# Performance work log

Measured on AMD Instinct MI355X. Metric: run time of the kernel, lower is better.

Reference implementation:

```python
import math
import jax, jax.numpy as jnp
import numpy as np

LMAX = 4
IN_FEATURES = 128
OUT_FEATURES = 128
BATCH = 16384
NUM_M = (LMAX + 1) ** 2  # 25


def setup_inputs() -> dict:
    key = jax.random.key(0)
    k1, k2 = jax.random.split(key)
    bound = 1.0 / math.sqrt(IN_FEATURES)
    input_embedding = jax.random.normal(k1, (BATCH, NUM_M, IN_FEATURES), dtype=jnp.float32)
    # Matches flax initializers.uniform(scale=2*bound): values in [0, 2*bound).
    # The module subtracts `bound` inside __call__, replicated in reference().
    weight = jax.random.uniform(k2, (LMAX + 1, OUT_FEATURES, IN_FEATURES),
                                dtype=jnp.float32, minval=0.0, maxval=2.0 * bound)
    bias = jnp.zeros((OUT_FEATURES,), dtype=jnp.float32)
    return {"input_embedding": input_embedding, "weight": weight, "bias": bias}


def reference(input_embedding, weight, bias):
    in_features = input_embedding.shape[-1]
    bound = 1.0 / math.sqrt(in_features)
    w = weight - bound  # centered weights, shape [lmax+1, out, in]
    lmax = weight.shape[0] - 1
    # expand_index[m] = l such that m lies in degree-l block (2l+1 entries each)
    expand_index = jnp.repeat(jnp.arange(lmax + 1), 2 * jnp.arange(lmax + 1) + 1,
                              total_repeat_length=(lmax + 1) ** 2)
    w_expanded = w[expand_index]  # [(lmax+1)^2, out, in] -- small gather
    out = jnp.einsum('bmi,moi->bmo', input_embedding, w_expanded)
    out = out.at[:, 0, :].add(bias)  # bias only on the l=0 (m=0) component
    return out
```

## Files before the change

kernel.cpp:

```cpp
#include <hip/hip_runtime.h>


#define BATCH 16384
#define NUM_M 25
#define NF 128
#define BB 64
#define ROWS_PER_BLOCK (BATCH / BB)
#define TILE_ROWS 64
#define NIT (ROWS_PER_BLOCK / TILE_ROWS)

typedef __attribute__((ext_vector_type(8))) short short8;
typedef __attribute__((ext_vector_type(4))) float floatx4;

__device__ inline short f2bf(float f) {
    union { float f; unsigned u; } v;
    v.f = f;
    unsigned r = v.u + 0x7fffu + ((v.u >> 16) & 1u);
    return (short)(r >> 16);
}

__device__ inline short8 cvt8(floatx4 x0, floatx4 x1) {
    short8 f;
    f[0] = f2bf(x0[0]); f[1] = f2bf(x0[1]);
    f[2] = f2bf(x0[2]); f[3] = f2bf(x0[3]);
    f[4] = f2bf(x1[0]); f[5] = f2bf(x1[1]);
    f[6] = f2bf(x1[2]); f[7] = f2bf(x1[3]);
    return f;
}

__global__ __launch_bounds__(256, 2)
void so3_mfma_kernel(const float* __restrict__ x,
                     const float* __restrict__ w,
                     const float* __restrict__ bias,
                     float* __restrict__ out) {
    const int m = blockIdx.y;
    const int l = (m >= 16) ? 4 : (m >= 9) ? 3 : (m >= 4) ? 2 : (m >= 1) ? 1 : 0;
    const int wave = threadIdx.x >> 6;
    const int lane = threadIdx.x & 63;
    const int q    = lane >> 4;
    const int n16  = lane & 15;
    const float bound = 0.08838834764831843f;

    short8 wfrag[8][4];
    {
        const float* wl = w + l * NF * NF;
        #pragma unroll
        for (int nt = 0; nt < 8; ++nt) {
            const int o = nt * 16 + n16;
            #pragma unroll
            for (int kc = 0; kc < 4; ++kc) {
                const int k = kc * 32 + q * 8;
                const floatx4* p = (const floatx4*)(wl + o * NF + k);
                floatx4 w0 = p[0], w1 = p[1];
                short8 f;
                f[0] = f2bf(w0[0] - bound); f[1] = f2bf(w0[1] - bound);
                f[2] = f2bf(w0[2] - bound); f[3] = f2bf(w0[3] - bound);
                f[4] = f2bf(w1[0] - bound); f[5] = f2bf(w1[1] - bound);
                f[6] = f2bf(w1[2] - bound); f[7] = f2bf(w1[3] - bound);
                wfrag[nt][kc] = f;
            }
        }
    }

    const int b0 = blockIdx.x * ROWS_PER_BLOCK;
    const int row0 = b0 + wave * 16 + n16;
    const float* xr0  = x   + (row0 * NUM_M + m) * NF;
    float*       or0  = out + (row0 * NUM_M + m) * NF;
    const int tile_stride = TILE_ROWS * NUM_M * NF;

    floatx4 raw[2][8];
    #pragma unroll
    for (int kc = 0; kc < 4; ++kc) {
        const floatx4* p = (const floatx4*)(xr0 + kc * 32 + q * 8);
        raw[0][2 * kc]     = p[0];
        raw[0][2 * kc + 1] = p[1];
    }

    #pragma unroll
    for (int it = 0; it < NIT; ++it) {
        const int cur = it & 1;

        if (it + 1 < NIT) {
            const float* xr = xr0 + (it + 1) * tile_stride;
            #pragma unroll
            for (int kc = 0; kc < 4; ++kc) {
                const floatx4* p = (const floatx4*)(xr + kc * 32 + q * 8);
                raw[cur ^ 1][2 * kc]     = p[0];
                raw[cur ^ 1][2 * kc + 1] = p[1];
            }
        }

        floatx4 acc[8] = {};
        #pragma unroll
        for (int kc = 0; kc < 4; ++kc) {
            const short8 a = cvt8(raw[cur][2 * kc], raw[cur][2 * kc + 1]);
            #pragma unroll
            for (int nt = 0; nt < 8; ++nt) {
                acc[nt] = __builtin_amdgcn_mfma_f32_16x16x32_bf16(
                    wfrag[nt][kc], a, acc[nt], 0, 0, 0);
            }
        }

        float* orow = or0 + it * tile_stride;
        #pragma unroll
        for (int nt = 0; nt < 8; ++nt) {
            floatx4 v = acc[nt];
            if (m == 0) {
                const floatx4 b4 = *(const floatx4*)(bias + nt * 16 + q * 4);
                v[0] += b4[0]; v[1] += b4[1]; v[2] += b4[2]; v[3] += b4[3];
            }
            __builtin_nontemporal_store(v, (floatx4*)(orow + nt * 16 + q * 4));
        }
    }
}

extern "C" void kernel_launch(void* const* d_in, const int* in_sizes, int n_in,
                              void* d_out, int out_size, void* d_ws, size_t ws_size,
                              hipStream_t stream) {
    const float* x    = (const float*)d_in[0];
    const float* w    = (const float*)d_in[1];
    const float* bias = (const float*)d_in[2];
    float* out = (float*)d_out;

    dim3 grid(BB, NUM_M);
    dim3 block(256);
    so3_mfma_kernel<<<grid, block, 0, stream>>>(x, w, bias, out);
}
```

Measured before the change: 416.7 us.

## Stage bf16 weights in swizzled LDS and raise occupancy to four blocks per SIMD

Weight fragments no longer live in registers (32 short8 per thread). Each block now converts its degree-l weight matrix to bf16 once into a 32KB XOR-swizzled LDS buffer and reads the fragments from LDS inside the MFMA loop. The x prefetch double buffer shrinks to a single raw buffer that is converted to bf16 fragments before the next load, and launch bounds go from 2 to 4. The aim is more waves in flight to hide the memory latency of this bandwidth-bound kernel, at the cost of LDS reads on every tile and a block-wide barrier.

```diff
diff --git a/kernel.cpp b/kernel.cpp
--- a/kernel.cpp
+++ b/kernel.cpp
@@ -28,77 +28,91 @@
     return f;
 }
 
-__global__ __launch_bounds__(256, 2)
+__global__ __launch_bounds__(256, 4)
 void so3_mfma_kernel(const float* __restrict__ x,
                      const float* __restrict__ w,
                      const float* __restrict__ bias,
                      float* __restrict__ out) {
+    __shared__ short wlds[NF * NF];
+
     const int m = blockIdx.y;
     const int l = (m >= 16) ? 4 : (m >= 9) ? 3 : (m >= 4) ? 2 : (m >= 1) ? 1 : 0;
-    const int wave = threadIdx.x >> 6;
-    const int lane = threadIdx.x & 63;
+    const int tid  = threadIdx.x;
+    const int wave = tid >> 6;
+    const int lane = tid & 63;
     const int q    = lane >> 4;
     const int n16  = lane & 15;
     const float bound = 0.08838834764831843f;
 
-    short8 wfrag[8][4];
-    {
-        const float* wl = w + l * NF * NF;
-        #pragma unroll
-        for (int nt = 0; nt < 8; ++nt) {
-            const int o = nt * 16 + n16;
-            #pragma unroll
-            for (int kc = 0; kc < 4; ++kc) {
-                const int k = kc * 32 + q * 8;
-                const floatx4* p = (const floatx4*)(wl + o * NF + k);
-                floatx4 w0 = p[0], w1 = p[1];
-                short8 f;
-                f[0] = f2bf(w0[0] - bound); f[1] = f2bf(w0[1] - bound);
-                f[2] = f2bf(w0[2] - bound); f[3] = f2bf(w0[3] - bound);
-                f[4] = f2bf(w1[0] - bound); f[5] = f2bf(w1[1] - bound);
-                f[6] = f2bf(w1[2] - bound); f[7] = f2bf(w1[3] - bound);
-                wfrag[nt][kc] = f;
-            }
-        }
-    }
-
-    const int b0 = blockIdx.x * ROWS_PER_BLOCK;
+    const int b0   = blockIdx.x * ROWS_PER_BLOCK;
     const int row0 = b0 + wave * 16 + n16;
-    const float* xr0  = x   + (row0 * NUM_M + m) * NF;
-    float*       or0  = out + (row0 * NUM_M + m) * NF;
+    const float* xr0 = x   + (row0 * NUM_M + m) * NF;
+    float*       or0 = out + (row0 * NUM_M + m) * NF;
     const int tile_stride = TILE_ROWS * NUM_M * NF;
 
-    floatx4 raw[2][8];
+    floatx4 raw[8];
     #pragma unroll
     for (int kc = 0; kc < 4; ++kc) {
         const floatx4* p = (const floatx4*)(xr0 + kc * 32 + q * 8);
-        raw[0][2 * kc]     = p[0];
-        raw[0][2 * kc + 1] = p[1];
+        raw[2 * kc]     = p[0];
+        raw[2 * kc + 1] = p[1];
     }
+
+    {
+        const int o    = tid >> 1;
+        const int half = tid & 1;
+        const float* wr = w + l * NF * NF + o * NF + half * 64;
+        char* wb = (char*)wlds;
+        #pragma unroll
+        for (int j = 0; j < 8; ++j) {
+            floatx4 f0 = ((const floatx4*)wr)[2 * j];
+            floatx4 f1 = ((const floatx4*)wr)[2 * j + 1];
+            short8 s;
+            s[0] = f2bf(f0[0] - bound); s[1] = f2bf(f0[1] - bound);
+            s[2] = f2bf(f0[2] - bound); s[3] = f2bf(f0[3] - bound);
+            s[4] = f2bf(f1[0] - bound); s[5] = f2bf(f1[1] - bound);
+            s[6] = f2bf(f1[2] - bound); s[7] = f2bf(f1[3] - bound);
+            const int c = half * 8 + j;
+            *(short8*)(wb + o * 256 + ((c * 16) ^ ((o & 7) << 4))) = s;
+        }
+    }
+    __syncthreads();
+
+    const char* wb = (const char*)wlds;
+    const int xm = (n16 & 7) << 4;
+    int lr[4];
+    #pragma unroll
+    for (int kc = 0; kc < 4; ++kc)
+        lr[kc] = n16 * 256 + ((kc * 64 + q * 16) ^ xm);
+
+    short8 afrag[4];
+    #pragma unroll
+    for (int kc = 0; kc < 4; ++kc)
+        afrag[kc] = cvt8(raw[2 * kc], raw[2 * kc + 1]);
 
     #pragma unroll
     for (int it = 0; it < NIT; ++it) {
-        const int cur = it & 1;
-
         if (it + 1 < NIT) {
             const float* xr = xr0 + (it + 1) * tile_stride;
             #pragma unroll
             for (int kc = 0; kc < 4; ++kc) {
                 const floatx4* p = (const floatx4*)(xr + kc * 32 + q * 8);
-                raw[cur ^ 1][2 * kc]     = p[0];
-                raw[cur ^ 1][2 * kc + 1] = p[1];
+                raw[2 * kc]     = p[0];
+                raw[2 * kc + 1] = p[1];
             }
         }
 
         floatx4 acc[8] = {};
         #pragma unroll
         for (int kc = 0; kc < 4; ++kc) {
-            const short8 a = cvt8(raw[cur][2 * kc], raw[cur][2 * kc + 1]);
+            short8 wt[8];
             #pragma unroll
-            for (int nt = 0; nt < 8; ++nt) {
+            for (int nt = 0; nt < 8; ++nt)
+                wt[nt] = *(const short8*)(wb + lr[kc] + nt * 4096);
+            #pragma unroll
+            for (int nt = 0; nt < 8; ++nt)
                 acc[nt] = __builtin_amdgcn_mfma_f32_16x16x32_bf16(
-                    wfrag[nt][kc], a, acc[nt], 0, 0, 0);
-            }
+                    wt[nt], afrag[kc], acc[nt], 0, 0, 0);
         }
 
         float* orow = or0 + it * tile_stride;
@@ -110,6 +124,12 @@
                 v[0] += b4[0]; v[1] += b4[1]; v[2] += b4[2]; v[3] += b4[3];
             }
             __builtin_nontemporal_store(v, (floatx4*)(orow + nt * 16 + q * 4));
+        }
+
+        if (it + 1 < NIT) {
+            #pragma unroll
+            for (int kc = 0; kc < 4; ++kc)
+                afrag[kc] = cvt8(raw[2 * kc], raw[2 * kc + 1]);
         }
     }
 }
```

New measurement: 396.1 us. 4.9% less time.
